# Performance work log

Hardware: AMD Instinct MI355X
Metric: run time of the kernel (lower is better)

## Reference

```python
import jax, jax.numpy as jnp
import numpy as np

SHRINK_THRES = 0.0025
R_THRES = 1.0
EPS = 1e-12


def setup_inputs() -> dict:
    key = jax.random.key(0)
    k1, k2 = jax.random.split(key)
    N, L, D = 16384, 4096, 1024  # samples, memory slots (lan_dim), fea_dim
    x = jax.random.normal(k1, (N, D), dtype=jnp.float32)
    stdv = 1.0 / np.sqrt(D)
    weight = jax.random.uniform(k2, (L, D), dtype=jnp.float32, minval=-stdv, maxval=stdv)
    return {"x": x, "weight": weight}


def reference(x, weight):
    # memory addressing: att = softmax(x @ W^T)  -> [N, L]
    att = jax.nn.softmax(x @ weight.T, axis=1)
    # hard_shrink_relu: relu(a - lambd) * a / (|a - lambd| + eps)
    shifted = att - SHRINK_THRES
    att = jax.nn.relu(shifted) * att / (jnp.abs(shifted) + EPS)
    # L1 normalize along dim 1 (F.normalize p=1, eps=1e-12)
    l1 = jnp.sum(jnp.abs(att), axis=1, keepdims=True)
    att = att / jnp.maximum(l1, EPS)
    # reconstruct from memory: [N, D]
    output = att @ weight
    # nearest landmark per sample (detached gather in original)
    ind = jnp.argmax(att, axis=1)                      # [N]
    nl = weight[ind]                                   # [N, D]
    # second-nearest: overwrite argmax slot with the row minimum, re-argmax
    rows = jnp.arange(att.shape[0])
    row_min = jnp.min(att, axis=1)
    att2 = att.at[rows, ind].set(row_min)
    ind2 = jnp.argmax(att2, axis=1)
    nl2 = weight[ind2]                                 # [N, D]
    # centroid-distance filter (original returns list of indices; we return a
    # jit-compatible boolean mask over samples instead)
    cen = jnp.mean(weight, axis=0)                     # [D]
    dist = jnp.sqrt(jnp.sum((x - cen) ** 2, axis=1))   # [N]
    col_mask = dist < R_THRES                          # [N] bool
    return (output, att, nl, nl2, col_mask)
```

## Files before the change

### kernel.cpp

```cpp
#include <hip/hip_runtime.h>
#include <cmath>

#define NS 16384
#define LS 4096
#define DF 1024
#define SHRINK_T 0.0025f
#define EPS_T 1e-12f

using f16 = _Float16;
using f16x4 = __attribute__((ext_vector_type(4))) _Float16;
using f16x8 = __attribute__((ext_vector_type(8))) _Float16;
using f32x16 = __attribute__((ext_vector_type(16))) float;

#define NSEG 64

__global__ void split_kernel(const float* __restrict__ src,
                             f16* __restrict__ hi, f16* __restrict__ lo, int n4) {
    int i = blockIdx.x * 256 + threadIdx.x;
    if (i >= n4) return;
    float4 v = reinterpret_cast<const float4*>(src)[i];
    f16x4 h, l;
    h[0] = (f16)v.x; h[1] = (f16)v.y; h[2] = (f16)v.z; h[3] = (f16)v.w;
    l[0] = (f16)(v.x - (float)h[0]);
    l[1] = (f16)(v.y - (float)h[1]);
    l[2] = (f16)(v.z - (float)h[2]);
    l[3] = (f16)(v.w - (float)h[3]);
    reinterpret_cast<f16x4*>(hi)[i] = h;
    reinterpret_cast<f16x4*>(lo)[i] = l;
}

__global__ void centroid_part_kernel(const float* __restrict__ w, float* __restrict__ part) {
    const int c = blockIdx.x * 256 + threadIdx.x;
    const int seg = blockIdx.y;
    const int l0 = seg * (LS / NSEG);
    float acc = 0.f;
    for (int l = 0; l < LS / NSEG; ++l)
        acc += w[(size_t)(l0 + l) * DF + c];
    part[(size_t)seg * DF + c] = acc;
}

__global__ void centroid_sum_kernel(const float* __restrict__ part, float* __restrict__ cen) {
    const int c = blockIdx.x * 256 + threadIdx.x;
    float acc = 0.f;
    for (int s = 0; s < NSEG; ++s) acc += part[(size_t)s * DF + c];
    cen[c] = acc * (1.0f / (float)LS);
}

#define BM 128
#define BN 128
#define BK 32

#define GLOAD16(gptr, lptr)                                                    \
    __builtin_amdgcn_global_load_lds(                                          \
        (const __attribute__((address_space(1))) void*)(gptr),                 \
        (__attribute__((address_space(3))) void*)(lptr), 16, 0, 0)

__device__ __forceinline__ int swz_s(int r) { return (r & 3) ^ ((r >> 2) & 1); }

__global__ __launch_bounds__(256) void gemm_f16_kernel(
    const f16* __restrict__ xh, const f16* __restrict__ xl,
    const f16* __restrict__ wh, const f16* __restrict__ wl,
    float* __restrict__ S, int r0, int rowsChunk)
{
    __shared__ __align__(16) f16 Ah[BM * BK];
    __shared__ __align__(16) f16 Al[BM * BK];
    __shared__ __align__(16) f16 Bh[BN * BK];
    __shared__ __align__(16) f16 Bl[BN * BK];

    const int t = threadIdx.x;
    const int lane = t & 63;
    const int wv = t >> 6;
    const int wr = (wv >> 1) * 64;
    const int wc = (wv & 1) * 64;
    const int rowBase = r0 + blockIdx.y * BM;
    const int colBase = blockIdx.x * BN;

    f32x16 acc[2][2];
#pragma unroll
    for (int m = 0; m < 2; ++m)
#pragma unroll
        for (int n = 0; n < 2; ++n)
#pragma unroll
            for (int j = 0; j < 16; ++j) acc[m][n][j] = 0.f;

    const int c32 = lane & 31;
    const int kh = lane >> 5;

    const int sr_lo = t >> 2;
    const int cc_lo = ((t & 3) ^ swz_s(sr_lo)) * 8;
    const int sr_hi = 64 + sr_lo;
    const int cc_hi = ((t & 3) ^ swz_s(sr_hi)) * 8;
    int ga_lo = rowBase + sr_lo; if (ga_lo >= NS) ga_lo = NS - 1;
    int ga_hi = rowBase + sr_hi; if (ga_hi >= NS) ga_hi = NS - 1;
    const size_t aoff_lo = (size_t)ga_lo * DF + cc_lo;
    const size_t aoff_hi = (size_t)ga_hi * DF + cc_hi;
    const size_t boff_lo = (size_t)(colBase + sr_lo) * DF + cc_lo;
    const size_t boff_hi = (size_t)(colBase + sr_hi) * DF + cc_hi;
    const int lb_lo = (wv * 16) * BK;
    const int lb_hi = (64 + wv * 16) * BK;

    for (int k0 = 0; k0 < DF; k0 += BK) {
        GLOAD16(xh + aoff_lo + k0, &Ah[lb_lo]);
        GLOAD16(xl + aoff_lo + k0, &Al[lb_lo]);
        GLOAD16(wh + boff_lo + k0, &Bh[lb_lo]);
        GLOAD16(wl + boff_lo + k0, &Bl[lb_lo]);
        GLOAD16(xh + aoff_hi + k0, &Ah[lb_hi]);
        GLOAD16(xl + aoff_hi + k0, &Al[lb_hi]);
        GLOAD16(wh + boff_hi + k0, &Bh[lb_hi]);
        GLOAD16(wl + boff_hi + k0, &Bl[lb_hi]);
        __syncthreads();

#pragma unroll
        for (int s = 0; s < 2; ++s) {
            f16x8 amh[2], aml[2], bnh[2], bnl[2];
#pragma unroll
            for (int m = 0; m < 2; ++m) {
                const int r = wr + m * 32 + c32;
                const int q = ((s * 2 + kh) ^ swz_s(r)) * 8;
                amh[m] = *(const f16x8*)&Ah[r * BK + q];
                aml[m] = *(const f16x8*)&Al[r * BK + q];
            }
#pragma unroll
            for (int n = 0; n < 2; ++n) {
                const int c = wc + n * 32 + c32;
                const int q = ((s * 2 + kh) ^ swz_s(c)) * 8;
                bnh[n] = *(const f16x8*)&Bh[c * BK + q];
                bnl[n] = *(const f16x8*)&Bl[c * BK + q];
            }
#pragma unroll
            for (int m = 0; m < 2; ++m)
#pragma unroll
                for (int n = 0; n < 2; ++n) {
                    acc[m][n] = __builtin_amdgcn_mfma_f32_32x32x16_f16(amh[m], bnh[n], acc[m][n], 0, 0, 0);
                    acc[m][n] = __builtin_amdgcn_mfma_f32_32x32x16_f16(amh[m], bnl[n], acc[m][n], 0, 0, 0);
                    acc[m][n] = __builtin_amdgcn_mfma_f32_32x32x16_f16(aml[m], bnh[n], acc[m][n], 0, 0, 0);
                }
        }
        __syncthreads();
    }

#pragma unroll
    for (int m = 0; m < 2; ++m) {
        const int rb = blockIdx.y * BM + wr + m * 32 + 4 * kh;
#pragma unroll
        for (int n = 0; n < 2; ++n) {
            const int cc = colBase + wc + n * 32 + c32;
#pragma unroll
            for (int reg = 0; reg < 16; ++reg) {
                const int rr = rb + (reg & 3) + 8 * (reg >> 2);
                if (rr < rowsChunk)
                    S[(size_t)rr * LS + cc] = acc[m][n][reg];
            }
        }
    }
}

__global__ __launch_bounds__(256) void pass2_kernel(
    const float* __restrict__ S, const float* __restrict__ x,
    const float* __restrict__ w, const float* __restrict__ cen,
    float* __restrict__ out, int r0)
{
    constexpr int T = 256;
    __shared__ __align__(16) float att_lds[LS];
    __shared__ float red[T];
    __shared__ int redi[T];

    const int t = threadIdx.x;
    const size_t row = (size_t)r0 + blockIdx.x;
    const float4* s4 = (const float4*)(S + (size_t)blockIdx.x * (size_t)LS);

    float* const out_output = out;
    float* const out_att  = out + (size_t)NS * DF;
    float* const out_nl   = out + (size_t)NS * DF + (size_t)NS * LS;
    float* const out_nl2  = out + (size_t)2 * NS * DF + (size_t)NS * LS;
    float* const out_mask = out + (size_t)3 * NS * DF + (size_t)NS * LS;

    float sv[16];
    float mx = -INFINITY;
#pragma unroll
    for (int i = 0; i < 4; ++i) {
        float4 v = s4[i * 256 + t];
        sv[i * 4 + 0] = v.x; sv[i * 4 + 1] = v.y;
        sv[i * 4 + 2] = v.z; sv[i * 4 + 3] = v.w;
        mx = fmaxf(mx, fmaxf(fmaxf(v.x, v.y), fmaxf(v.z, v.w)));
    }
    red[t] = mx;
    __syncthreads();
    for (int off = 128; off >= 1; off >>= 1) {
        if (t < off) red[t] = fmaxf(red[t], red[t + off]);
        __syncthreads();
    }
    const float m = red[0];
    __syncthreads();

    float zs = 0.f;
#pragma unroll
    for (int i = 0; i < 16; ++i) {
        sv[i] = expf(sv[i] - m);
        zs += sv[i];
    }
    red[t] = zs;
    __syncthreads();
    for (int off = 128; off >= 1; off >>= 1) {
        if (t < off) red[t] += red[t + off];
        __syncthreads();
    }
    const float Z = red[0];
    __syncthreads();

    float l1 = 0.f;
#pragma unroll
    for (int i = 0; i < 16; ++i) {
        float a = sv[i] / Z;
        float r = a - SHRINK_T;
        float v = (r > 0.f) ? (r * a) / (r + EPS_T) : 0.f;
        sv[i] = v;
        l1 += v;
    }
    red[t] = l1;
    __syncthreads();
    for (int off = 128; off >= 1; off >>= 1) {
        if (t < off) red[t] += red[t + off];
        __syncthreads();
    }
    const float nrm = fmaxf(red[0], EPS_T);
    __syncthreads();

    float bv = -INFINITY; int bi = LS;
    float mn = INFINITY;
    float4* const attl4 = (float4*)att_lds;
    float4* const att4o = (float4*)(out_att + row * LS);
#pragma unroll
    for (int i = 0; i < 4; ++i) {
        float4 vn4;
        vn4.x = sv[i * 4 + 0] / nrm; vn4.y = sv[i * 4 + 1] / nrm;
        vn4.z = sv[i * 4 + 2] / nrm; vn4.w = sv[i * 4 + 3] / nrm;
        sv[i * 4 + 0] = vn4.x; sv[i * 4 + 1] = vn4.y;
        sv[i * 4 + 2] = vn4.z; sv[i * 4 + 3] = vn4.w;
        attl4[i * 256 + t] = vn4;
        att4o[i * 256 + t] = vn4;
#pragma unroll
        for (int c = 0; c < 4; ++c) {
            const float v = sv[i * 4 + c];
            const int j = i * 1024 + 4 * t + c;
            if (v > bv) { bv = v; bi = j; }
            mn = fminf(mn, v);
        }
    }
    __syncthreads();

    red[t] = bv; redi[t] = bi;
    __syncthreads();
    for (int off = 128; off >= 1; off >>= 1) {
        if (t < off) {
            float ov = red[t + off]; int oi = redi[t + off];
            if (ov > red[t] || (ov == red[t] && oi < redi[t])) { red[t] = ov; redi[t] = oi; }
        }
        __syncthreads();
    }
    const int ind = redi[0];
    __syncthreads();

    red[t] = mn;
    __syncthreads();
    for (int off = 128; off >= 1; off >>= 1) {
        if (t < off) red[t] = fminf(red[t], red[t + off]);
        __syncthreads();
    }
    const float rowmin = red[0];
    __syncthreads();

    bv = -INFINITY; bi = LS;
#pragma unroll
    for (int i = 0; i < 4; ++i)
#pragma unroll
        for (int c = 0; c < 4; ++c) {
            const int j = i * 1024 + 4 * t + c;
            const float vv = (j == ind) ? rowmin : sv[i * 4 + c];
            if (vv > bv) { bv = vv; bi = j; }
        }
    red[t] = bv; redi[t] = bi;
    __syncthreads();
    for (int off = 128; off >= 1; off >>= 1) {
        if (t < off) {
            float ov = red[t + off]; int oi = redi[t + off];
            if (ov > red[t] || (ov == red[t] && oi < redi[t])) { red[t] = ov; redi[t] = oi; }
        }
        __syncthreads();
    }
    const int ind2 = redi[0];
    __syncthreads();

    const int lane = t & 63;
    float4 oa = {0.f, 0.f, 0.f, 0.f};
    for (int k0 = 0; k0 < LS; k0 += 64) {
        float av = att_lds[k0 + lane];
        unsigned long long msk = __ballot(av > 0.f);
        while (msk) {
            int b = __ffsll((unsigned long long)msk) - 1;
            msk &= msk - 1;
            float vv = att_lds[k0 + b];
            float4 wv4 = ((const float4*)(w + (size_t)(k0 + b) * DF))[t];
            oa.x = fmaf(vv, wv4.x, oa.x);
            oa.y = fmaf(vv, wv4.y, oa.y);
            oa.z = fmaf(vv, wv4.z, oa.z);
            oa.w = fmaf(vv, wv4.w, oa.w);
        }
    }
    ((float4*)(out_output + row * DF))[t] = oa;

    ((float4*)(out_nl  + row * DF))[t] = ((const float4*)(w + (size_t)ind  * DF))[t];
    ((float4*)(out_nl2 + row * DF))[t] = ((const float4*)(w + (size_t)ind2 * DF))[t];

    float4 xv = ((const float4*)(x + row * DF))[t];
    float4 cv = ((const float4*)cen)[t];
    float ds = 0.f;
    ds = fmaf(xv.x - cv.x, xv.x - cv.x, ds);
    ds = fmaf(xv.y - cv.y, xv.y - cv.y, ds);
    ds = fmaf(xv.z - cv.z, xv.z - cv.z, ds);
    ds = fmaf(xv.w - cv.w, xv.w - cv.w, ds);
    red[t] = ds;
    __syncthreads();
    for (int off = 128; off >= 1; off >>= 1) {
        if (t < off) red[t] += red[t + off];
        __syncthreads();
    }
    if (t == 0) {
        float dist = sqrtf(red[0]);
        out_mask[row] = (dist < 1.0f) ? 1.0f : 0.0f;
    }
}

extern "C" void kernel_launch(void* const* d_in, const int* in_sizes, int n_in,
                              void* d_out, int out_size, void* d_ws, size_t ws_size,
                              hipStream_t stream)
{
    const float* x = (const float*)d_in[0];
    const float* w = (const float*)d_in[1];
    float* out = (float*)d_out;

    float* cen = (float*)d_ws;
    float* part = cen + DF;
    f16* xh = (f16*)(part + (size_t)NSEG * DF);
    f16* xl = xh + (size_t)NS * DF;
    f16* wh = xl + (size_t)NS * DF;
    f16* wl = wh + (size_t)LS * DF;
    float* S = (float*)(wl + (size_t)LS * DF);

    const size_t head_bytes = sizeof(float) * (DF + (size_t)NSEG * DF)
                            + (size_t)2 * 2 * NS * DF + (size_t)2 * 2 * LS * DF;
    long cap_rows = (long)((ws_size - head_bytes) / (sizeof(float) * LS));
    if (cap_rows > NS) cap_rows = NS;
    if (cap_rows < 1) cap_rows = 1;
    int chunk = (cap_rows >= BM) ? (int)(cap_rows - (cap_rows % BM)) : (int)cap_rows;

    centroid_part_kernel<<<dim3(DF / 256, NSEG), 256, 0, stream>>>(w, part);
    centroid_sum_kernel<<<DF / 256, 256, 0, stream>>>(part, cen);
    split_kernel<<<(NS * DF / 4 + 255) / 256, 256, 0, stream>>>(x, xh, xl, NS * DF / 4);
    split_kernel<<<(LS * DF / 4 + 255) / 256, 256, 0, stream>>>(w, wh, wl, LS * DF / 4);

    for (int r0 = 0; r0 < NS; r0 += chunk) {
        int rows = (NS - r0 < chunk) ? (NS - r0) : chunk;
        dim3 grid((LS + BN - 1) / BN, (rows + BM - 1) / BM);
        gemm_f16_kernel<<<grid, 256, 0, stream>>>(xh, xl, wh, wl, S, r0, rows);
        pass2_kernel<<<rows, 256, 0, stream>>>(S, x, w, cen, out, r0);
    }
}
```

Measured before the change: 596.5 us.

## Double-buffer GEMM LDS tiles with larger 256x128 block tile and capped chunk

```diff
diff --git a/kernel.cpp b/kernel.cpp
--- a/kernel.cpp
+++ b/kernel.cpp
@@ -46,105 +46,102 @@
     cen[c] = acc * (1.0f / (float)LS);
 }
 
-#define BM 128
+#define BM 256
 #define BN 128
-#define BK 32
+#define BK 16
+#define NKT (DF / BK)
 
 #define GLOAD16(gptr, lptr)                                                    \
     __builtin_amdgcn_global_load_lds(                                          \
         (const __attribute__((address_space(1))) void*)(gptr),                 \
         (__attribute__((address_space(3))) void*)(lptr), 16, 0, 0)
 
-__device__ __forceinline__ int swz_s(int r) { return (r & 3) ^ ((r >> 2) & 1); }
-
-__global__ __launch_bounds__(256) void gemm_f16_kernel(
+__global__ __launch_bounds__(256, 2) void gemm_f16_kernel(
     const f16* __restrict__ xh, const f16* __restrict__ xl,
     const f16* __restrict__ wh, const f16* __restrict__ wl,
     float* __restrict__ S, int r0, int rowsChunk)
 {
-    __shared__ __align__(16) f16 Ah[BM * BK];
-    __shared__ __align__(16) f16 Al[BM * BK];
-    __shared__ __align__(16) f16 Bh[BN * BK];
-    __shared__ __align__(16) f16 Bl[BN * BK];
+    __shared__ __align__(16) f16 Ah[2][BM * BK];
+    __shared__ __align__(16) f16 Al[2][BM * BK];
+    __shared__ __align__(16) f16 Bh[2][BN * BK];
+    __shared__ __align__(16) f16 Bl[2][BN * BK];
 
     const int t = threadIdx.x;
     const int lane = t & 63;
     const int wv = t >> 6;
-    const int wr = (wv >> 1) * 64;
-    const int wc = (wv & 1) * 64;
     const int rowBase = r0 + blockIdx.y * BM;
     const int colBase = blockIdx.x * BN;
 
-    f32x16 acc[2][2];
+    f32x16 acc[2][4];
 #pragma unroll
     for (int m = 0; m < 2; ++m)
 #pragma unroll
-        for (int n = 0; n < 2; ++n)
+        for (int n = 0; n < 4; ++n)
 #pragma unroll
             for (int j = 0; j < 16; ++j) acc[m][n][j] = 0.f;
 
     const int c32 = lane & 31;
     const int kh = lane >> 5;
 
-    const int sr_lo = t >> 2;
-    const int cc_lo = ((t & 3) ^ swz_s(sr_lo)) * 8;
-    const int sr_hi = 64 + sr_lo;
-    const int cc_hi = ((t & 3) ^ swz_s(sr_hi)) * 8;
-    int ga_lo = rowBase + sr_lo; if (ga_lo >= NS) ga_lo = NS - 1;
-    int ga_hi = rowBase + sr_hi; if (ga_hi >= NS) ga_hi = NS - 1;
-    const size_t aoff_lo = (size_t)ga_lo * DF + cc_lo;
-    const size_t aoff_hi = (size_t)ga_hi * DF + cc_hi;
-    const size_t boff_lo = (size_t)(colBase + sr_lo) * DF + cc_lo;
-    const size_t boff_hi = (size_t)(colBase + sr_hi) * DF + cc_hi;
-    const int lb_lo = (wv * 16) * BK;
-    const int lb_hi = (64 + wv * 16) * BK;
-
-    for (int k0 = 0; k0 < DF; k0 += BK) {
-        GLOAD16(xh + aoff_lo + k0, &Ah[lb_lo]);
-        GLOAD16(xl + aoff_lo + k0, &Al[lb_lo]);
-        GLOAD16(wh + boff_lo + k0, &Bh[lb_lo]);
-        GLOAD16(wl + boff_lo + k0, &Bl[lb_lo]);
-        GLOAD16(xh + aoff_hi + k0, &Ah[lb_hi]);
-        GLOAD16(xl + aoff_hi + k0, &Al[lb_hi]);
-        GLOAD16(wh + boff_hi + k0, &Bh[lb_hi]);
-        GLOAD16(wl + boff_hi + k0, &Bl[lb_hi]);
-        __syncthreads();
-
-#pragma unroll
-        for (int s = 0; s < 2; ++s) {
-            f16x8 amh[2], aml[2], bnh[2], bnl[2];
-#pragma unroll
-            for (int m = 0; m < 2; ++m) {
-                const int r = wr + m * 32 + c32;
-                const int q = ((s * 2 + kh) ^ swz_s(r)) * 8;
-                amh[m] = *(const f16x8*)&Ah[r * BK + q];
-                aml[m] = *(const f16x8*)&Al[r * BK + q];
+    const int srow = t >> 1;
+    const int sc = (t & 1) * 8;
+    int ga0 = rowBase + srow;        if (ga0 >= NS) ga0 = NS - 1;
+    int ga1 = rowBase + 128 + srow;  if (ga1 >= NS) ga1 = NS - 1;
+    const size_t aoff0 = (size_t)ga0 * DF + sc;
+    const size_t aoff1 = (size_t)ga1 * DF + sc;
+    const size_t boff  = (size_t)(colBase + srow) * DF + sc;
+    const int lbA0 = wv * 512;
+    const int lbA1 = 2048 + wv * 512;
+    const int lbB  = wv * 512;
+
+#define STAGE(k0, b)                                      \
+    do {                                                  \
+        GLOAD16(xh + aoff0 + (k0), &Ah[b][lbA0]);         \
+        GLOAD16(xl + aoff0 + (k0), &Al[b][lbA0]);         \
+        GLOAD16(xh + aoff1 + (k0), &Ah[b][lbA1]);         \
+        GLOAD16(xl + aoff1 + (k0), &Al[b][lbA1]);         \
+        GLOAD16(wh + boff  + (k0), &Bh[b][lbB]);          \
+        GLOAD16(wl + boff  + (k0), &Bl[b][lbB]);          \
+    } while (0)
+
+    const int baseA = (wv * 64 + c32) * BK + kh * 8;
+    const int baseB = c32 * BK + kh * 8;
+
+    STAGE(0, 0);
+
+    for (int kt = 0; kt < NKT; ++kt) {
+        const int b = kt & 1;
+        __syncthreads();
+        if (kt + 1 < NKT) STAGE((kt + 1) * BK, b ^ 1);
+
+        f16x8 amh[2], aml[2], bnh[4], bnl[4];
+#pragma unroll
+        for (int m = 0; m < 2; ++m) {
+            amh[m] = *(const f16x8*)&Ah[b][baseA + m * 32 * BK];
+            aml[m] = *(const f16x8*)&Al[b][baseA + m * 32 * BK];
+        }
+#pragma unroll
+        for (int n = 0; n < 4; ++n) {
+            bnh[n] = *(const f16x8*)&Bh[b][baseB + n * 32 * BK];
+            bnl[n] = *(const f16x8*)&Bl[b][baseB + n * 32 * BK];
+        }
+#pragma unroll
+        for (int m = 0; m < 2; ++m)
+#pragma unroll
+            for (int n = 0; n < 4; ++n) {
+                acc[m][n] = __builtin_amdgcn_mfma_f32_32x32x16_f16(amh[m], bnh[n], acc[m][n], 0, 0, 0);
+                acc[m][n] = __builtin_amdgcn_mfma_f32_32x32x16_f16(amh[m], bnl[n], acc[m][n], 0, 0, 0);
+                acc[m][n] = __builtin_amdgcn_mfma_f32_32x32x16_f16(aml[m], bnh[n], acc[m][n], 0, 0, 0);
             }
-#pragma unroll
-            for (int n = 0; n < 2; ++n) {
-                const int c = wc + n * 32 + c32;
-                const int q = ((s * 2 + kh) ^ swz_s(c)) * 8;
-                bnh[n] = *(const f16x8*)&Bh[c * BK + q];
-                bnl[n] = *(const f16x8*)&Bl[c * BK + q];
-            }
-#pragma unroll
-            for (int m = 0; m < 2; ++m)
-#pragma unroll
-                for (int n = 0; n < 2; ++n) {
-                    acc[m][n] = __builtin_amdgcn_mfma_f32_32x32x16_f16(amh[m], bnh[n], acc[m][n], 0, 0, 0);
-                    acc[m][n] = __builtin_amdgcn_mfma_f32_32x32x16_f16(amh[m], bnl[n], acc[m][n], 0, 0, 0);
-                    acc[m][n] = __builtin_amdgcn_mfma_f32_32x32x16_f16(aml[m], bnh[n], acc[m][n], 0, 0, 0);
-                }
-        }
-        __syncthreads();
-    }
+    }
+#undef STAGE
 
 #pragma unroll
     for (int m = 0; m < 2; ++m) {
-        const int rb = blockIdx.y * BM + wr + m * 32 + 4 * kh;
-#pragma unroll
-        for (int n = 0; n < 2; ++n) {
-            const int cc = colBase + wc + n * 32 + c32;
+        const int rb = blockIdx.y * BM + wv * 64 + m * 32 + 4 * kh;
+#pragma unroll
+        for (int n = 0; n < 4; ++n) {
+            const int cc = colBase + n * 32 + c32;
 #pragma unroll
             for (int reg = 0; reg < 16; ++reg) {
                 const int rr = rb + (reg & 3) + 8 * (reg >> 2);
@@ -352,7 +349,9 @@
     long cap_rows = (long)((ws_size - head_bytes) / (sizeof(float) * LS));
     if (cap_rows > NS) cap_rows = NS;
     if (cap_rows < 1) cap_rows = 1;
-    int chunk = (cap_rows >= BM) ? (int)(cap_rows - (cap_rows % BM)) : (int)cap_rows;
+    long want = 4096;
+    long pick = (cap_rows < want) ? cap_rows : want;
+    int chunk = (pick >= BM) ? (int)(pick - (pick % BM)) : (int)pick;
 
     centroid_part_kernel<<<dim3(DF / 256, NSEG), 256, 0, stream>>>(w, part);
     centroid_sum_kernel<<<DF / 256, 256, 0, stream>>>(part, cen);
```

New measurement: 768.7 us. +28.9%, slower.
